# Kernel tuning notes

Hardware: AMD Instinct MI355X
Metric: run time of the kernel (lower is better)

Reference implementation:

```python
import jax, jax.numpy as jnp
import numpy as np

T, E, H, K, WCNT, L = 131072, 512, 512, 1024, 50000, 128
NUM_LAYERS = 1


def setup_inputs() -> dict:
    key = jax.random.key(0)
    ks = jax.random.split(key, 12)
    f32 = jnp.float32
    return {
        "topic": jax.random.randint(ks[0], (L,), 0, WCNT, dtype=jnp.int32),
        "score_s": jax.random.uniform(ks[1], (1,), dtype=f32),
        "emb": jax.random.normal(ks[2], (WCNT, E), dtype=f32) * 0.05,
        "h": jax.random.normal(ks[3], (NUM_LAYERS, 1, H), dtype=f32) * 0.05,
        "vs": jax.random.normal(ks[4], (T, E), dtype=f32) * 0.05,
        "hs": jax.random.normal(ks[5], (T, 1, H), dtype=f32) * 0.05,
        "w_ih": jax.random.normal(ks[6], (3 * H, 2 * E + 1), dtype=f32) * 0.02,
        "w_hh": jax.random.normal(ks[7], (3 * H, H), dtype=f32) * 0.02,
        "b_ih": jnp.zeros((3 * H,), f32),
        "b_hh": jnp.zeros((3 * H,), f32),
        "w_score": jax.random.normal(ks[8], (1, E + 2 * H + 1), dtype=f32) * 0.02,
        "b_score": jnp.zeros((1,), f32),
    }


def _forward(topic, score_s, emb, h, vs, hs, w_ih, w_hh, b_ih, b_hh, w_score, b_score):
    # topic embedding: mean of word vectors -> v [E]
    v = emb[topic].mean(axis=0)
    # dot-product attention over growing history
    alpha = vs @ v                               # [T]
    vals, idx = jax.lax.top_k(alpha, K)          # top-k similar past items
    a = jax.nn.softmax(vals)                     # [K]
    hs_flat = hs.reshape(-1, NUM_LAYERS * H)     # [T, H]
    attn_h = a @ hs_flat[idx]                    # [H] weighted combine of gathered states
    length = jnp.full((1,), K, dtype=v.dtype)
    # with_last=True: cat([v, attn_h, h, length])
    pred_v = jnp.concatenate([v, attn_h, h.reshape(-1), length])[None, :]  # [1, E+2H+1]
    score = pred_v @ w_score.T + b_score         # [1, 1]
    # score_mode='double': split v by correctness of s
    pos = (score_s >= 0.5).astype(v.dtype)[0]
    x = jnp.concatenate([v * pos, v * (1.0 - pos), score_s])  # [2E+1]
    # single GRU step (torch gate layout: r, z, n)
    h_prev = h.reshape(H)
    gi = w_ih @ x + b_ih
    gh = w_hh @ h_prev + b_hh
    r = jax.nn.sigmoid(gi[:H] + gh[:H])
    z = jax.nn.sigmoid(gi[H:2 * H] + gh[H:2 * H])
    n = jnp.tanh(gi[2 * H:] + r * gh[2 * H:])
    h_new = ((1.0 - z) * n + z * h_prev).reshape(NUM_LAYERS, 1, H)
    # LSTMA updates the history
    vs_new = jnp.concatenate([vs, v[None, :]], axis=0)
    hs_new = jnp.concatenate([hs, h_new], axis=0)
    return score, h_new, vs_new, hs_new


def reference(topic, score_s, emb, h, vs, hs, w_ih, w_hh, b_ih, b_hh, w_score, b_score):
    return _forward(topic, score_s, emb, h, vs, hs, w_ih, w_hh, b_ih, b_hh, w_score, b_score)
```

## Files before the change

### kernel.cpp

```cpp
#include <hip/hip_runtime.h>
#include <math.h>

constexpr int T_ = 131072;
constexpr int E_ = 512;
constexpr int H_ = 512;
constexpr int K_ = 1024;
constexpr int L_ = 128;

typedef __attribute__((ext_vector_type(4))) float f32x4;

constexpr size_t OFF_V     = 0;
constexpr size_t OFF_ALPHA = 512;
constexpr size_t OFF_HIST1 = OFF_ALPHA + T_;
constexpr size_t OFF_HIST2 = OFF_HIST1 + 65536;
constexpr size_t OFF_CNT   = OFF_HIST2 + 65536;
constexpr size_t OFF_INFO  = OFF_CNT + 2;
constexpr size_t OFF_VALS  = OFF_INFO + 8;
constexpr size_t OFF_IDX   = OFF_VALS + K_;
constexpr size_t OFF_GI    = OFF_IDX + K_;
constexpr size_t OFF_GH    = OFF_GI + 3 * H_;

constexpr int ZERO_N = 65536 + 65536 + 2;

constexpr size_t OUT_VS = 513;
constexpr size_t OUT_HS = 513 + (size_t)(T_ + 1) * E_;

constexpr int NB_GRU = 384;


__device__ __forceinline__ unsigned fkey(float f) {
    unsigned u = __float_as_uint(f);
    return (u & 0x80000000u) ? ~u : (u | 0x80000000u);
}

__global__ __launch_bounds__(1024) void k_init(const int* __restrict__ topic,
                                               const float* __restrict__ emb,
                                               float* __restrict__ ws_v,
                                               unsigned* __restrict__ zero_base,
                                               float* __restrict__ out) {
    if (blockIdx.x == gridDim.x - 1) {
        __shared__ float part[512];
        int t = threadIdx.x;
        int e = t & 511, g = t >> 9;
        float s = 0.f;
        #pragma unroll 8
        for (int l = g * 64; l < g * 64 + 64; ++l) {
            int tp = topic[l];
            s += emb[(size_t)tp * E_ + e];
        }
        if (g == 1) part[e] = s;
        __syncthreads();
        if (g == 0) {
            float v = (s + part[e]) * (1.0f / L_);
            ws_v[e] = v;
            out[OUT_VS + (size_t)T_ * E_ + e] = v;
        }
    } else {
        int i = blockIdx.x * blockDim.x + threadIdx.x;
        if (i < ZERO_N) zero_base[i] = 0u;
    }
}

__global__ __launch_bounds__(256) void k_mega(const float* __restrict__ vs,
                                              const float* __restrict__ hs,
                                              const float* __restrict__ ws_v,
                                              float* __restrict__ alpha,
                                              unsigned* __restrict__ hist1,
                                              const float* __restrict__ wih,
                                              const float* __restrict__ whh,
                                              const float* __restrict__ bih,
                                              const float* __restrict__ bhh,
                                              const float* __restrict__ score_s,
                                              const float* __restrict__ h_in,
                                              float* __restrict__ gi,
                                              float* __restrict__ gh,
                                              float* __restrict__ out) {
    __shared__ float x[1025 + 512];
    int t = threadIdx.x;
    int wave = t >> 6, lane = t & 63;
    int b = blockIdx.x;
    if (b < NB_GRU) {
        float ss = score_s[0];
        float pos = ss >= 0.5f ? 1.f : 0.f;
        for (int c = t; c < 1025; c += 256) {
            float xv;
            if (c < 512)       xv = ws_v[c] * pos;
            else if (c < 1024) xv = ws_v[c - 512] * (1.f - pos);
            else               xv = ss;
            x[c] = xv;
        }
        for (int c = t; c < 512; c += 256) x[1025 + c] = h_in[c];
        __syncthreads();
        int row = b * 4 + wave;
        const float* wr = wih + (size_t)row * 1025;
        float s1 = 0.f;
        for (int c = lane; c < 1025; c += 64) s1 = fmaf(wr[c], x[c], s1);
        const float* hr = whh + (size_t)row * 512;
        float s2 = 0.f;
        #pragma unroll
        for (int c = lane; c < 512; c += 64) s2 = fmaf(hr[c], x[1025 + c], s2);
        #pragma unroll
        for (int m = 32; m; m >>= 1) {
            s1 += __shfl_xor(s1, m, 64);
            s2 += __shfl_xor(s2, m, 64);
        }
        if (lane == 0) { gi[row] = s1 + bih[row]; gh[row] = s2 + bhh[row]; }
        return;
    }
    b -= NB_GRU;
    bool is_vs = b < (T_ / 4);
    int row = (is_vs ? b : b - T_ / 4) * 4 + wave;
    const f32x4* src4 = (const f32x4*)((is_vs ? vs : hs) + (size_t)row * E_);
    f32x4 a0 = __builtin_nontemporal_load(&src4[lane]);
    f32x4 a1 = __builtin_nontemporal_load(&src4[lane + 64]);
    if (is_vs) {
        const f32x4* v4 = (const f32x4*)ws_v;
        f32x4 b0 = v4[lane];
        f32x4 b1 = v4[lane + 64];
        float dot = 0.f;
        dot = fmaf(a0.x, b0.x, dot); dot = fmaf(a0.y, b0.y, dot);
        dot = fmaf(a0.z, b0.z, dot); dot = fmaf(a0.w, b0.w, dot);
        dot = fmaf(a1.x, b1.x, dot); dot = fmaf(a1.y, b1.y, dot);
        dot = fmaf(a1.z, b1.z, dot); dot = fmaf(a1.w, b1.w, dot);
        #pragma unroll
        for (int m = 32; m; m >>= 1) dot += __shfl_xor(dot, m, 64);
        if (lane == 0) {
            alpha[row] = dot;
            atomicAdd(&hist1[fkey(dot) >> 16], 1u);
        }
    }
    int nl = (lane + 1) & 63;
    float n0x = __shfl(a0.x, nl, 64), n0y = __shfl(a0.y, nl, 64), n0z = __shfl(a0.z, nl, 64);
    float n1x = __shfl(a1.x, nl, 64), n1y = __shfl(a1.y, nl, 64), n1z = __shfl(a1.z, nl, 64);
    float* dst = out + (is_vs ? OUT_VS : OUT_HS) + (size_t)row * E_;
    f32x4* d4 = (f32x4*)(dst + 3);
    bool last = (lane == 63);
    f32x4 lo;
    lo.x = a0.w;
    lo.y = last ? n1x : n0x;
    lo.z = last ? n1y : n0y;
    lo.w = last ? n1z : n0z;
    __builtin_nontemporal_store(lo, &d4[lane]);
    if (!last) {
        f32x4 hi;
        hi.x = a1.w; hi.y = n1x; hi.z = n1y; hi.w = n1z;
        __builtin_nontemporal_store(hi, &d4[lane + 64]);
    }
    if (lane == 0) { dst[0] = a0.x; dst[1] = a0.y; dst[2] = a0.z; }
    if (last) dst[511] = a1.w;
}

__global__ __launch_bounds__(256) void k_scan(const unsigned* __restrict__ hist,
                                              unsigned* __restrict__ info, int pass) {
    __shared__ unsigned ps[256];
    __shared__ unsigned s_chunk, s_above;
    int t = threadIdx.x;
    unsigned Kwant = (pass == 0) ? (unsigned)K_ : ((unsigned)K_ - info[1]);
    unsigned base = 65536u - (unsigned)(t + 1) * 256u;
    unsigned s = 0;
    for (int j = 0; j < 256; ++j) s += hist[base + j];
    ps[t] = s;
    __syncthreads();
    #pragma unroll
    for (int off = 1; off < 256; off <<= 1) {
        unsigned v = (t >= off) ? ps[t - off] : 0u;
        __syncthreads();
        ps[t] += v;
        __syncthreads();
    }
    unsigned incl = ps[t], excl = incl - s;
    if (excl < Kwant && incl >= Kwant) { s_chunk = (unsigned)t; s_above = excl; }
    __syncthreads();
    unsigned c = s_chunk;
    unsigned Kw2 = Kwant - s_above;
    unsigned bin = 65535u - c * 256u - (unsigned)t;
    unsigned b = hist[bin];
    __syncthreads();
    ps[t] = b;
    __syncthreads();
    #pragma unroll
    for (int off = 1; off < 256; off <<= 1) {
        unsigned v = (t >= off) ? ps[t - off] : 0u;
        __syncthreads();
        ps[t] += v;
        __syncthreads();
    }
    unsigned inc2 = ps[t], ex2 = inc2 - b;
    if (ex2 < Kw2 && inc2 >= Kw2) {
        unsigned cnt_above = s_above + ex2;
        if (pass == 0) { info[0] = bin; info[1] = cnt_above; }
        else {
            info[2] = (info[0] << 16) | bin;
            info[3] = info[1] + cnt_above;
            info[4] = (unsigned)K_ - info[3];
        }
    }
}

__global__ __launch_bounds__(256) void k_hist2(const float* __restrict__ alpha,
                                               const unsigned* __restrict__ info,
                                               unsigned* __restrict__ hist2) {
    int i = blockIdx.x * blockDim.x + threadIdx.x;
    unsigned key = fkey(alpha[i]);
    if ((key >> 16) == info[0]) atomicAdd(&hist2[key & 0xFFFFu], 1u);
}

__global__ __launch_bounds__(256) void k_select(const float* __restrict__ alpha,
                                                const unsigned* __restrict__ info,
                                                unsigned* __restrict__ cnt,
                                                float* __restrict__ vals,
                                                int* __restrict__ idx) {
    int i = blockIdx.x * blockDim.x + threadIdx.x;
    float a = alpha[i];
    unsigned key = fkey(a);
    unsigned thr = info[2];
    if (key > thr) {
        unsigned p = atomicAdd(&cnt[0], 1u);
        vals[p] = a; idx[p] = i;
    } else if (key == thr) {
        unsigned t = atomicAdd(&cnt[1], 1u);
        if (t < info[4]) {
            unsigned p = info[3] + t;
            vals[p] = a; idx[p] = i;
        }
    }
}

__global__ __launch_bounds__(512) void k_attn(const float* __restrict__ hs,
                                              const float* __restrict__ vals,
                                              const int* __restrict__ idx,
                                              float* __restrict__ part) {
    __shared__ float red[512];
    int t = threadIdx.x, j = blockIdx.x;
    float v0 = vals[t], v1 = vals[t + 512];
    red[t] = fmaxf(v0, v1);
    __syncthreads();
    for (int s = 256; s > 0; s >>= 1) { if (t < s) red[t] = fmaxf(red[t], red[t + s]); __syncthreads(); }
    float m = red[0];
    __syncthreads();
    red[t] = expf(v0 - m) + expf(v1 - m);
    __syncthreads();
    for (int s = 256; s > 0; s >>= 1) { if (t < s) red[t] += red[t + s]; __syncthreads(); }
    float S = red[0];
    float acc = 0.f;
    #pragma unroll
    for (int k = j * 8; k < j * 8 + 8; ++k) {
        float w = expf(vals[k] - m) / S;
        acc = fmaf(w, hs[(size_t)idx[k] * E_ + t], acc);
    }
    part[(size_t)j * E_ + t] = acc;
}

__global__ __launch_bounds__(512) void k_final(const float* __restrict__ gi,
                                               const float* __restrict__ gh,
                                               const float* __restrict__ h_in,
                                               const float* __restrict__ part,
                                               const float* __restrict__ ws_v,
                                               const float* __restrict__ w_score,
                                               const float* __restrict__ b_score,
                                               float* __restrict__ out) {
    __shared__ float red[512];
    int j = threadIdx.x;
    float r = 1.f / (1.f + expf(-(gi[j] + gh[j])));
    float z = 1.f / (1.f + expf(-(gi[H_ + j] + gh[H_ + j])));
    float n = tanhf(gi[2 * H_ + j] + r * gh[2 * H_ + j]);
    float hp = h_in[j];
    float hn = (1.f - z) * n + z * hp;
    out[1 + j] = hn;
    out[OUT_HS + (size_t)T_ * E_ + j] = hn;
    float attn = 0.f;
    for (int jj = 0; jj < 128; ++jj) attn += part[(size_t)jj * E_ + j];
    float d = ws_v[j] * w_score[j] + attn * w_score[512 + j] + hp * w_score[1024 + j];
    if (j == 0) d += 1024.0f * w_score[1536] + b_score[0];
    red[j] = d;
    __syncthreads();
    for (int s = 256; s > 0; s >>= 1) { if (j < s) red[j] += red[j + s]; __syncthreads(); }
    if (j == 0) out[0] = red[0];
}

extern "C" void kernel_launch(void* const* d_in, const int* in_sizes, int n_in,
                              void* d_out, int out_size, void* d_ws, size_t ws_size,
                              hipStream_t stream) {
    const int*   topic   = (const int*)d_in[0];
    const float* score_s = (const float*)d_in[1];
    const float* emb     = (const float*)d_in[2];
    const float* h_in    = (const float*)d_in[3];
    const float* vs      = (const float*)d_in[4];
    const float* hs      = (const float*)d_in[5];
    const float* w_ih    = (const float*)d_in[6];
    const float* w_hh    = (const float*)d_in[7];
    const float* b_ih    = (const float*)d_in[8];
    const float* b_hh    = (const float*)d_in[9];
    const float* w_score = (const float*)d_in[10];
    const float* b_score = (const float*)d_in[11];
    float* out = (float*)d_out;

    float*    wsf   = (float*)d_ws;
    float*    v_ws  = wsf + OFF_V;
    float*    alpha = wsf + OFF_ALPHA;
    unsigned* hist1 = (unsigned*)(wsf + OFF_HIST1);
    unsigned* hist2 = (unsigned*)(wsf + OFF_HIST2);
    unsigned* cnt   = (unsigned*)(wsf + OFF_CNT);
    unsigned* info  = (unsigned*)(wsf + OFF_INFO);
    float*    vals  = wsf + OFF_VALS;
    int*      idx   = (int*)(wsf + OFF_IDX);
    float*    part  = wsf + OFF_ALPHA;
    float*    gi    = wsf + OFF_GI;
    float*    gh    = wsf + OFF_GH;

    hipLaunchKernelGGL(k_init, dim3(130), dim3(1024), 0, stream,
                       topic, emb, v_ws, hist1, out);
    hipLaunchKernelGGL(k_mega, dim3(NB_GRU + 2 * (T_ / 4)), dim3(256), 0, stream,
                       vs, hs, v_ws, alpha, hist1,
                       w_ih, w_hh, b_ih, b_hh, score_s, h_in, gi, gh, out);
    hipLaunchKernelGGL(k_scan, dim3(1), dim3(256), 0, stream, hist1, info, 0);
    hipLaunchKernelGGL(k_hist2, dim3(T_ / 256), dim3(256), 0, stream, alpha, info, hist2);
    hipLaunchKernelGGL(k_scan, dim3(1), dim3(256), 0, stream, hist2, info, 1);
    hipLaunchKernelGGL(k_select, dim3(T_ / 256), dim3(256), 0, stream, alpha, info, cnt, vals, idx);
    hipLaunchKernelGGL(k_attn, dim3(128), dim3(512), 0, stream, hs, vals, idx, part);
    hipLaunchKernelGGL(k_final, dim3(1), dim3(512), 0, stream,
                       gi, gh, h_in, part, v_ws, w_score, b_score, out);
}
```

Baseline: 235.8 us.

## Replace second radix pass with candidate collection and rank-based resolve

Top-k selection previously made a second 16-bit histogram pass plus a second scan over all alpha values. It now collects candidates that fall in the boundary top-16-bit bin into a buffer. A single-block kernel then ranks them by O(n^2) comparison to fill the remaining slots. This removes one full pass over alpha, one launch and the zeroing of the second histogram. The trade-off is a serial quadratic resolve that becomes slow if the boundary bin holds many candidates, and correctness is lost if more than the buffer capacity of candidates land in it.

```diff
diff --git a/kernel.cpp b/kernel.cpp
--- a/kernel.cpp
+++ b/kernel.cpp
@@ -6,21 +6,23 @@
 constexpr int H_ = 512;
 constexpr int K_ = 1024;
 constexpr int L_ = 128;
+constexpr int CAND_CAP = 16384;
 
 typedef __attribute__((ext_vector_type(4))) float f32x4;
 
 constexpr size_t OFF_V     = 0;
 constexpr size_t OFF_ALPHA = 512;
 constexpr size_t OFF_HIST1 = OFF_ALPHA + T_;
-constexpr size_t OFF_HIST2 = OFF_HIST1 + 65536;
-constexpr size_t OFF_CNT   = OFF_HIST2 + 65536;
+constexpr size_t OFF_CNT   = OFF_HIST1 + 65536;
 constexpr size_t OFF_INFO  = OFF_CNT + 2;
 constexpr size_t OFF_VALS  = OFF_INFO + 8;
 constexpr size_t OFF_IDX   = OFF_VALS + K_;
-constexpr size_t OFF_GI    = OFF_IDX + K_;
+constexpr size_t OFF_CANDV = OFF_IDX + K_;
+constexpr size_t OFF_CANDI = OFF_CANDV + CAND_CAP;
+constexpr size_t OFF_GI    = OFF_CANDI + CAND_CAP;
 constexpr size_t OFF_GH    = OFF_GI + 3 * H_;
 
-constexpr int ZERO_N = 65536 + 65536 + 2;
+constexpr int ZERO_N = 65536 + 2;
 
 constexpr size_t OUT_VS = 513;
 constexpr size_t OUT_HS = 513 + (size_t)(T_ + 1) * E_;
@@ -151,11 +153,11 @@
 }
 
 __global__ __launch_bounds__(256) void k_scan(const unsigned* __restrict__ hist,
-                                              unsigned* __restrict__ info, int pass) {
+                                              unsigned* __restrict__ info) {
     __shared__ unsigned ps[256];
     __shared__ unsigned s_chunk, s_above;
     int t = threadIdx.x;
-    unsigned Kwant = (pass == 0) ? (unsigned)K_ : ((unsigned)K_ - info[1]);
+    unsigned Kwant = (unsigned)K_;
     unsigned base = 65536u - (unsigned)(t + 1) * 256u;
     unsigned s = 0;
     for (int j = 0; j < 256; ++j) s += hist[base + j];
@@ -187,42 +189,50 @@
     }
     unsigned inc2 = ps[t], ex2 = inc2 - b;
     if (ex2 < Kw2 && inc2 >= Kw2) {
-        unsigned cnt_above = s_above + ex2;
-        if (pass == 0) { info[0] = bin; info[1] = cnt_above; }
-        else {
-            info[2] = (info[0] << 16) | bin;
-            info[3] = info[1] + cnt_above;
-            info[4] = (unsigned)K_ - info[3];
-        }
-    }
-}
-
-__global__ __launch_bounds__(256) void k_hist2(const float* __restrict__ alpha,
-                                               const unsigned* __restrict__ info,
-                                               unsigned* __restrict__ hist2) {
-    int i = blockIdx.x * blockDim.x + threadIdx.x;
-    unsigned key = fkey(alpha[i]);
-    if ((key >> 16) == info[0]) atomicAdd(&hist2[key & 0xFFFFu], 1u);
-}
-
-__global__ __launch_bounds__(256) void k_select(const float* __restrict__ alpha,
-                                                const unsigned* __restrict__ info,
-                                                unsigned* __restrict__ cnt,
-                                                float* __restrict__ vals,
-                                                int* __restrict__ idx) {
+        info[0] = bin;
+        info[1] = s_above + ex2;
+    }
+}
+
+__global__ __launch_bounds__(256) void k_collect(const float* __restrict__ alpha,
+                                                 const unsigned* __restrict__ info,
+                                                 unsigned* __restrict__ cnt,
+                                                 float* __restrict__ vals,
+                                                 int* __restrict__ idx,
+                                                 float* __restrict__ candv,
+                                                 int* __restrict__ candi) {
     int i = blockIdx.x * blockDim.x + threadIdx.x;
     float a = alpha[i];
-    unsigned key = fkey(a);
-    unsigned thr = info[2];
-    if (key > thr) {
+    unsigned hb = fkey(a) >> 16;
+    unsigned bin1 = info[0];
+    if (hb > bin1) {
         unsigned p = atomicAdd(&cnt[0], 1u);
         vals[p] = a; idx[p] = i;
-    } else if (key == thr) {
-        unsigned t = atomicAdd(&cnt[1], 1u);
-        if (t < info[4]) {
-            unsigned p = info[3] + t;
-            vals[p] = a; idx[p] = i;
-        }
+    } else if (hb == bin1) {
+        unsigned q = atomicAdd(&cnt[1], 1u);
+        if (q < (unsigned)CAND_CAP) { candv[q] = a; candi[q] = i; }
+    }
+}
+
+__global__ __launch_bounds__(256) void k_resolve(const float* __restrict__ candv,
+                                                 const int* __restrict__ candi,
+                                                 const unsigned* __restrict__ cnt,
+                                                 float* __restrict__ vals,
+                                                 int* __restrict__ idx) {
+    int t = threadIdx.x;
+    unsigned nc = cnt[1] < (unsigned)CAND_CAP ? cnt[1] : (unsigned)CAND_CAP;
+    unsigned ndef = cnt[0];
+    unsigned k2 = (unsigned)K_ - ndef;
+    for (unsigned i = t; i < nc; i += 256) {
+        unsigned ki = fkey(candv[i]);
+        unsigned greater = 0, eqb = 0;
+        for (unsigned j = 0; j < nc; ++j) {
+            unsigned kj = fkey(candv[j]);
+            greater += (kj > ki) ? 1u : 0u;
+            eqb += (kj == ki && j < i) ? 1u : 0u;
+        }
+        unsigned r = greater + eqb;
+        if (r < k2) { vals[ndef + r] = candv[i]; idx[ndef + r] = candi[i]; }
     }
 }
 
@@ -299,24 +309,26 @@
     float*    v_ws  = wsf + OFF_V;
     float*    alpha = wsf + OFF_ALPHA;
     unsigned* hist1 = (unsigned*)(wsf + OFF_HIST1);
-    unsigned* hist2 = (unsigned*)(wsf + OFF_HIST2);
     unsigned* cnt   = (unsigned*)(wsf + OFF_CNT);
     unsigned* info  = (unsigned*)(wsf + OFF_INFO);
     float*    vals  = wsf + OFF_VALS;
     int*      idx   = (int*)(wsf + OFF_IDX);
+    float*    candv = wsf + OFF_CANDV;
+    int*      candi = (int*)(wsf + OFF_CANDI);
     float*    part  = wsf + OFF_ALPHA;
     float*    gi    = wsf + OFF_GI;
     float*    gh    = wsf + OFF_GH;
 
-    hipLaunchKernelGGL(k_init, dim3(130), dim3(1024), 0, stream,
+    hipLaunchKernelGGL(k_init, dim3(66), dim3(1024), 0, stream,
                        topic, emb, v_ws, hist1, out);
     hipLaunchKernelGGL(k_mega, dim3(NB_GRU + 2 * (T_ / 4)), dim3(256), 0, stream,
                        vs, hs, v_ws, alpha, hist1,
                        w_ih, w_hh, b_ih, b_hh, score_s, h_in, gi, gh, out);
-    hipLaunchKernelGGL(k_scan, dim3(1), dim3(256), 0, stream, hist1, info, 0);
-    hipLaunchKernelGGL(k_hist2, dim3(T_ / 256), dim3(256), 0, stream, alpha, info, hist2);
-    hipLaunchKernelGGL(k_scan, dim3(1), dim3(256), 0, stream, hist2, info, 1);
-    hipLaunchKernelGGL(k_select, dim3(T_ / 256), dim3(256), 0, stream, alpha, info, cnt, vals, idx);
+    hipLaunchKernelGGL(k_scan, dim3(1), dim3(256), 0, stream, hist1, info);
+    hipLaunchKernelGGL(k_collect, dim3(T_ / 256), dim3(256), 0, stream,
+                       alpha, info, cnt, vals, idx, candv, candi);
+    hipLaunchKernelGGL(k_resolve, dim3(1), dim3(256), 0, stream,
+                       candv, candi, cnt, vals, idx);
     hipLaunchKernelGGL(k_attn, dim3(128), dim3(512), 0, stream, hs, vals, idx, part);
     hipLaunchKernelGGL(k_final, dim3(1), dim3(512), 0, stream,
                        gi, gh, h_in, part, v_ws, w_score, b_score, out);
```

Measured after the change: 227.6 us. 3.5% less time.
